# Kernel tuning notes

Measured on AMD Instinct MI355X. Metric: run time of the kernel, lower is better.

## Reference

```python
import jax, jax.numpy as jnp
import numpy as np

B, N, E, ITERS = 8, 1024, 10, 5


def _xavier(key, shape):
    fan_in, fan_out = shape[1], shape[0]
    std = float(np.sqrt(2.0 / (fan_in + fan_out)))
    return jax.random.normal(key, shape, dtype=jnp.float32) * std


def setup_inputs() -> dict:
    key = jax.random.key(0)
    ks = jax.random.split(key, 10)
    return {
        "features": jax.random.uniform(ks[0], (B, N), dtype=jnp.float32),
        "weights": jax.random.uniform(ks[1], (B, N, N), dtype=jnp.float32),
        "adjacency": jax.random.uniform(ks[2], (B, N, N), dtype=jnp.float32),
        # torch Linear(in, out) weight has shape (out, in); y = x @ W.T
        "w_selected": _xavier(ks[3], (E, 1)),
        "w_nbpriors": _xavier(ks[4], (E, E)),
        "w_nbweights": _xavier(ks[5], (E, E)),
        "w_nbweights_ew": _xavier(ks[6], (E, 1)),
        "w_q_reduc": _xavier(ks[7], (1, 2 * E)),
        "w_q_allembed": _xavier(ks[8], (E, E)),
        "w_q_action": _xavier(ks[9], (E, E)),
    }


def reference(features, weights, adjacency, w_selected, w_nbpriors,
              w_nbweights, w_nbweights_ew, w_q_reduc, w_q_allembed, w_q_action):
    b, n = features.shape
    e = w_selected.shape[0]
    # v_selected = Linear(1,E)(features[...,None]) -> outer product with (E,) vector
    v_selected = features[:, :, None] * w_selected[:, 0]            # [B,N,E]
    # relu(Linear(1,E)(weights[...,None])), then sum over dim=1 (source nodes)
    w_exp = jax.nn.relu(weights[:, :, :, None] * w_nbweights_ew[:, 0])  # [B,N,N,E]
    v_weights = jnp.einsum('bje,fe->bjf', jnp.sum(w_exp, axis=1), w_nbweights)  # [B,N,E]
    base = v_selected + v_weights

    embeddings = jnp.zeros((b, n, e), dtype=features.dtype)
    for _ in range(ITERS):
        v_priors = jnp.einsum('bij,bje->bie', adjacency, embeddings)  # [B,N,E]
        v_priors = jnp.einsum('bie,fe->bif', v_priors, w_nbpriors)
        embeddings = jax.nn.relu(base + v_priors)

    sumembed = jnp.einsum('bne,fe->bf', embeddings, w_q_allembed)     # [B,E]
    sumembed = jnp.broadcast_to(sumembed[:, None, :], (b, n, e))
    peract = jnp.einsum('bne,fe->bnf', embeddings, w_q_action)        # [B,N,E]
    q_in = jnp.concatenate([sumembed, peract], axis=2)                # [B,N,2E]
    q_vals = jnp.einsum('bnk,ok->bno', q_in, w_q_reduc)[:, :, 0]      # [B,N]
    return q_vals, embeddings
```

## Files before the change

kernel.cpp:

```cpp
#include <hip/hip_runtime.h>

#define B 8
#define N 1024
#define E 10
#define GP 44
#define EMB_FLOATS (256 * GP)
#define EMB_F4 (EMB_FLOATS / 4)
#define NBLK 256
#define TPB 32
#define BAR_PAD 32

typedef float f32x4 __attribute__((ext_vector_type(4)));

__device__ __forceinline__ void batch_barrier(unsigned* cnt) {
    __syncthreads();
    if (threadIdx.x == 0) {
        __hip_atomic_fetch_add(cnt, 1u, __ATOMIC_RELAXED, __HIP_MEMORY_SCOPE_AGENT);
        while (__hip_atomic_load(cnt, __ATOMIC_RELAXED, __HIP_MEMORY_SCOPE_AGENT) < TPB)
            __builtin_amdgcn_s_sleep(2);
    }
    __syncthreads();
    asm volatile("" ::: "memory");
}

__device__ __forceinline__ void store_llc(float* p, float v) {
    __hip_atomic_store((unsigned*)p, __float_as_uint(v),
                       __ATOMIC_RELAXED, __HIP_MEMORY_SCOPE_AGENT);
}
__device__ __forceinline__ float load_llc(const float* p) {
    unsigned u = __hip_atomic_load((const unsigned*)p,
                                   __ATOMIC_RELAXED, __HIP_MEMORY_SCOPE_AGENT);
    return __uint_as_float(u);
}


__global__ __launch_bounds__(1024, 4)
void k_fused6(
    const float* __restrict__ W, const float* __restrict__ features,
    const float* __restrict__ w_sel, const float* __restrict__ w_nbw,
    const float* __restrict__ w_ew, const float* __restrict__ A,
    const float* __restrict__ Wp, const float* __restrict__ w_reduc,
    const float* __restrict__ w_all, const float* __restrict__ w_act,
    float* eA, float* eB,
    float* __restrict__ emb_out, float* __restrict__ qv,
    float* __restrict__ qpart, unsigned* __restrict__ bars)
{
    __shared__ float4 EmS[EMB_F4];
    __shared__ float vred[16][9][2 * E];
    __shared__ float WpS[E * E];
    __shared__ float gaS[E], gactS[E];
    __shared__ float vS[32 * E], qS[32 * E], qrow[32];
    __shared__ float qsumS;

    int bx = blockIdx.x, tid = threadIdx.x;
    int b = bx >> 5, tile = bx & 31;
    int i0 = tile * 32;
    int m = tid >> 6;
    int s = tid & 63;
    unsigned* mybars = bars + b * BAR_PAD;

    float Arf[2][4][4];
    {
        const float* Ab = A + ((size_t)(b * N) + i0 + m) * N + 4 * s;
#pragma unroll
        for (int k = 0; k < 2; ++k)
#pragma unroll
            for (int c = 0; c < 4; ++c) {
                float4 t = *(const float4*)(Ab + (size_t)(16 * k) * N + 256 * c);
                Arf[k][c][0] = t.x; Arf[k][c][1] = t.y;
                Arf[k][c][2] = t.z; Arf[k][c][3] = t.w;
            }
    }

    if (tid < E * E) WpS[tid] = Wp[tid];
    if (tid < E) {
        float sa = 0.f, sc = 0.f;
#pragma unroll
        for (int k = 0; k < E; ++k) {
            sa += w_reduc[k] * w_all[k * E + tid];
            sc += w_reduc[E + k] * w_act[k * E + tid];
        }
        gaS[tid] = sa;
        gactS[tid] = sc;
    }

    float b_reg = 0.f;
    {
        float* redPt = (float*)&EmS[0];
        float* redNt = redPt + 32 * 129;
        float* scol  = redNt + 32 * 129;
        int c4 = (tid & 7) * 4;
        int rg = tid >> 3;
        const float* wp = W + ((size_t)b * N + rg * 8) * N + i0 + c4;
        float4 sp = {0.f, 0.f, 0.f, 0.f}, sn = {0.f, 0.f, 0.f, 0.f};
#pragma unroll
        for (int i = 0; i < 8; ++i) {
            float4 ww = *(const float4*)(wp + (size_t)i * N);
            sp.x += fmaxf(ww.x, 0.f); sn.x += fmaxf(-ww.x, 0.f);
            sp.y += fmaxf(ww.y, 0.f); sn.y += fmaxf(-ww.y, 0.f);
            sp.z += fmaxf(ww.z, 0.f); sn.z += fmaxf(-ww.z, 0.f);
            sp.w += fmaxf(ww.w, 0.f); sn.w += fmaxf(-ww.w, 0.f);
        }
        redPt[(c4 + 0) * 129 + rg] = sp.x; redNt[(c4 + 0) * 129 + rg] = sn.x;
        redPt[(c4 + 1) * 129 + rg] = sp.y; redNt[(c4 + 1) * 129 + rg] = sn.y;
        redPt[(c4 + 2) * 129 + rg] = sp.z; redNt[(c4 + 2) * 129 + rg] = sn.z;
        redPt[(c4 + 3) * 129 + rg] = sp.w; redNt[(c4 + 3) * 129 + rg] = sn.w;
        __syncthreads();
        if (tid < 64) {
            int cc = tid & 31;
            const float* rp = (tid < 32) ? redPt : redNt;
            float t = 0.f;
#pragma unroll 8
            for (int g = 0; g < 128; ++g) t += rp[cc * 129 + g];
            scol[(tid >> 5) * 32 + cc] = t;
        }
        __syncthreads();
        if (tid < 32 * E) {
            int cc = tid / E, f = tid % E;
            float spc = scol[cc], snc = scol[32 + cc];
            float acc = features[(b << 10) + i0 + cc] * w_sel[f];
#pragma unroll
            for (int e = 0; e < E; ++e) {
                float ce = w_ew[e];
                float se = (ce > 0.f) ? ce * spc : (-ce) * snc;
                acc += w_nbw[f * E + e] * se;
            }
            b_reg = acc;
            int row = i0 + cc;
            store_llc(&eA[(size_t)b * EMB_FLOATS + (row >> 2) * GP + (row & 3) * E + f],
                      fmaxf(acc, 0.f));
        }
    }
    batch_barrier(&mybars[0]);

    float da = 0.f;
    for (int it = 0; it < 4; ++it) {
        const float* ein = (it & 1) ? (const float*)eB : (const float*)eA;
        float* eout = (it & 1) ? eA : eB;

        {
            const f32x4* src = (const f32x4*)ein + (size_t)b * EMB_F4;
            f32x4 t0, t1, t2 = {0.f, 0.f, 0.f, 0.f};
            asm volatile("global_load_dwordx4 %0, %1, off sc0 sc1"
                         : "=v"(t0) : "v"(src + tid) : "memory");
            asm volatile("global_load_dwordx4 %0, %1, off sc0 sc1"
                         : "=v"(t1) : "v"(src + tid + 1024) : "memory");
            if (tid < EMB_F4 - 2048)
                asm volatile("global_load_dwordx4 %0, %1, off sc0 sc1"
                             : "=v"(t2) : "v"(src + tid + 2048) : "memory");
            asm volatile("s_waitcnt vmcnt(0)" ::: "memory");
            __builtin_amdgcn_sched_barrier(0);
            ((f32x4*)EmS)[tid]        = t0;
            ((f32x4*)EmS)[tid + 1024] = t1;
            if (tid < EMB_F4 - 2048) ((f32x4*)EmS)[tid + 2048] = t2;
        }
        __syncthreads();

        float acc[2][E];
#pragma unroll
        for (int k = 0; k < 2; ++k)
#pragma unroll
            for (int e = 0; e < E; ++e) acc[k][e] = 0.f;

#pragma unroll
        for (int c = 0; c < 4; ++c) {
            float4 g4[10];
            const float4* gp = EmS + (size_t)(s + 64 * c) * (GP / 4);
#pragma unroll
            for (int t = 0; t < 10; ++t) g4[t] = gp[t];
            const float* g40 = (const float*)g4;
#pragma unroll
            for (int q = 0; q < 4; ++q)
#pragma unroll
                for (int k = 0; k < 2; ++k) {
                    float a = Arf[k][c][q];
#pragma unroll
                    for (int e = 0; e < E; ++e)
                        acc[k][e] += a * g40[q * E + e];
                }
        }

#pragma unroll
        for (int mask = 1; mask <= 4; mask <<= 1)
#pragma unroll
            for (int k = 0; k < 2; ++k)
#pragma unroll
                for (int e = 0; e < E; ++e)
                    acc[k][e] += __shfl_xor(acc[k][e], mask, 64);
        if ((s & 7) == 0)
#pragma unroll
            for (int k = 0; k < 2; ++k)
#pragma unroll
                for (int e = 0; e < E; ++e)
                    vred[m][s >> 3][k * E + e] = acc[k][e];
        __syncthreads();

        if (tid < 32 * E) {
            int r = tid / E, f = tid % E;
            int mm = r & 15, kk = r >> 4;
            float v[E];
#pragma unroll
            for (int e = 0; e < E; ++e) {
                float t = 0.f;
#pragma unroll
                for (int g = 0; g < 8; ++g) t += vred[mm][g][kk * E + e];
                v[e] = t;
            }
            float d = 0.f;
#pragma unroll
            for (int e = 0; e < E; ++e) d += v[e] * WpS[f * E + e];
            float r_out = fmaxf(b_reg + d, 0.f);
            if (it < 3) {
                int grow = i0 + r;
                store_llc(&eout[(size_t)b * EMB_FLOATS + (grow >> 2) * GP + (grow & 3) * E + f],
                          r_out);
            } else {
                size_t gi = (size_t)((b << 10) + i0 + r);
                emb_out[gi * E + f] = r_out;
                vS[tid] = r_out * gactS[f];
                qS[tid] = r_out * gaS[f];
            }
        }
        if (it < 3) batch_barrier(&mybars[(1 + it) * B * BAR_PAD]);
    }

    __syncthreads();
    if (tid < 32) {
        float dg = 0.f;
#pragma unroll
        for (int f = 0; f < E; ++f) {
            da += vS[tid * E + f];
            dg += qS[tid * E + f];
        }
        qrow[tid] = dg;
    }
    __syncthreads();
    if (tid == 0) {
        float t = 0.f;
#pragma unroll
        for (int r = 0; r < 32; ++r) t += qrow[r];
        store_llc(&qpart[bx], t);
    }
    batch_barrier(&mybars[4 * B * BAR_PAD]);

    if (tid < 32) {
        float t = load_llc(&qpart[(b << 5) + tid]);
#pragma unroll
        for (int mask = 1; mask < 32; mask <<= 1)
            t += __shfl_xor(t, mask, 32);
        if (tid == 0) qsumS = t;
    }
    __syncthreads();
    if (tid < 32) qv[(b << 10) + i0 + tid] = da + qsumS;
}

__global__
__attribute__((amdgpu_flat_work_group_size(1024, 1024)))
__attribute__((amdgpu_waves_per_eu(4, 4)))
void k_fused7(
    const float* __restrict__ W, const float* __restrict__ features,
    const float* __restrict__ w_sel, const float* __restrict__ w_nbw,
    const float* __restrict__ w_ew, const float* __restrict__ A,
    const float* __restrict__ Wp, const float* __restrict__ w_reduc,
    const float* __restrict__ w_all, const float* __restrict__ w_act,
    float* eA, float* eB,
    float* __restrict__ emb_out, float* __restrict__ qv,
    float* __restrict__ qpart, unsigned* __restrict__ bars)
{
    __shared__ float4 EmS[EMB_F4];
    __shared__ float vred[16][5][4 * E];
    __shared__ float WpS[E * E];
    __shared__ float gaS[E], gactS[E];
    __shared__ float vS[32 * E], qS[32 * E], qrow[32];
    __shared__ float qsumS;

    int bx = blockIdx.x, tid = threadIdx.x;
    int b = bx >> 5, tile = bx & 31;
    int i0 = tile * 32;
    int w = tid >> 6;
    int s = tid & 63;
    int rs = tid >> 7;
    int jg = tid & 127;
    unsigned* mybars = bars + b * BAR_PAD;

    float Arf[4][2][4];
    {
        const float* Ab = A + ((size_t)(b * N) + i0 + (rs << 2)) * N + 4 * jg;
#pragma unroll
        for (int rr = 0; rr < 4; ++rr)
#pragma unroll
            for (int c = 0; c < 2; ++c) {
                float4 t = *(const float4*)(Ab + (size_t)rr * N + 512 * c);
                Arf[rr][c][0] = t.x; Arf[rr][c][1] = t.y;
                Arf[rr][c][2] = t.z; Arf[rr][c][3] = t.w;
            }
    }

    if (tid < E * E) WpS[tid] = Wp[tid];
    if (tid < E) {
        float sa = 0.f, sc = 0.f;
#pragma unroll
        for (int k = 0; k < E; ++k) {
            sa += w_reduc[k] * w_all[k * E + tid];
            sc += w_reduc[E + k] * w_act[k * E + tid];
        }
        gaS[tid] = sa;
        gactS[tid] = sc;
    }

    float b_reg = 0.f;
    {
        float* redPt = (float*)&EmS[0];
        float* redNt = redPt + 32 * 129;
        float* scol  = redNt + 32 * 129;
        int c4 = (tid & 7) * 4;
        int rg = tid >> 3;
        const float* wp = W + ((size_t)b * N + rg * 8) * N + i0 + c4;
        float4 sp = {0.f, 0.f, 0.f, 0.f}, sn = {0.f, 0.f, 0.f, 0.f};
#pragma unroll
        for (int i = 0; i < 8; ++i) {
            float4 ww = *(const float4*)(wp + (size_t)i * N);
            sp.x += fmaxf(ww.x, 0.f); sn.x += fmaxf(-ww.x, 0.f);
            sp.y += fmaxf(ww.y, 0.f); sn.y += fmaxf(-ww.y, 0.f);
            sp.z += fmaxf(ww.z, 0.f); sn.z += fmaxf(-ww.z, 0.f);
            sp.w += fmaxf(ww.w, 0.f); sn.w += fmaxf(-ww.w, 0.f);
        }
        redPt[(c4 + 0) * 129 + rg] = sp.x; redNt[(c4 + 0) * 129 + rg] = sn.x;
        redPt[(c4 + 1) * 129 + rg] = sp.y; redNt[(c4 + 1) * 129 + rg] = sn.y;
        redPt[(c4 + 2) * 129 + rg] = sp.z; redNt[(c4 + 2) * 129 + rg] = sn.z;
        redPt[(c4 + 3) * 129 + rg] = sp.w; redNt[(c4 + 3) * 129 + rg] = sn.w;
        __syncthreads();
        if (tid < 64) {
            int cc = tid & 31;
            const float* rp = (tid < 32) ? redPt : redNt;
            float t = 0.f;
#pragma unroll 8
            for (int g = 0; g < 128; ++g) t += rp[cc * 129 + g];
            scol[(tid >> 5) * 32 + cc] = t;
        }
        __syncthreads();
        if (tid < 32 * E) {
            int cc = tid / E, f = tid % E;
            float spc = scol[cc], snc = scol[32 + cc];
            float acc = features[(b << 10) + i0 + cc] * w_sel[f];
#pragma unroll
            for (int e = 0; e < E; ++e) {
                float ce = w_ew[e];
                float se = (ce > 0.f) ? ce * spc : (-ce) * snc;
                acc += w_nbw[f * E + e] * se;
            }
            b_reg = acc;
            int row = i0 + cc;
            store_llc(&eA[(size_t)b * EMB_FLOATS + (row >> 2) * GP + (row & 3) * E + f],
                      fmaxf(acc, 0.f));
        }
    }
    batch_barrier(&mybars[0]);

    float da = 0.f;
    for (int it = 0; it < 4; ++it) {
        const float* ein = (it & 1) ? (const float*)eB : (const float*)eA;
        float* eout = (it & 1) ? eA : eB;

        {
            const f32x4* src = (const f32x4*)ein + (size_t)b * EMB_F4;
            f32x4 t0, t1, t2 = {0.f, 0.f, 0.f, 0.f};
            asm volatile("global_load_dwordx4 %0, %1, off sc0 sc1"
                         : "=v"(t0) : "v"(src + tid) : "memory");
            asm volatile("global_load_dwordx4 %0, %1, off sc0 sc1"
                         : "=v"(t1) : "v"(src + tid + 1024) : "memory");
            if (tid < EMB_F4 - 2048)
                asm volatile("global_load_dwordx4 %0, %1, off sc0 sc1"
                             : "=v"(t2) : "v"(src + tid + 2048) : "memory");
            asm volatile("s_waitcnt vmcnt(0)" ::: "memory");
            __builtin_amdgcn_sched_barrier(0);
            ((f32x4*)EmS)[tid]        = t0;
            ((f32x4*)EmS)[tid + 1024] = t1;
            if (tid < EMB_F4 - 2048) ((f32x4*)EmS)[tid + 2048] = t2;
        }
        __syncthreads();

        float acc[4][E];
#pragma unroll
        for (int rr = 0; rr < 4; ++rr)
#pragma unroll
            for (int e = 0; e < E; ++e) acc[rr][e] = 0.f;

#pragma unroll
        for (int c = 0; c < 2; ++c) {
            const float4* gp = EmS + (size_t)(jg + 128 * c) * (GP / 4);
            {
                float4 g4a[5];
#pragma unroll
                for (int t = 0; t < 5; ++t) g4a[t] = gp[t];
                const float* ga = (const float*)g4a;
#pragma unroll
                for (int q = 0; q < 2; ++q)
#pragma unroll
                    for (int rr = 0; rr < 4; ++rr) {
                        float a = Arf[rr][c][q];
#pragma unroll
                        for (int e = 0; e < E; ++e)
                            acc[rr][e] += a * ga[q * E + e];
                    }
            }
            {
                float4 g4b[5];
#pragma unroll
                for (int t = 0; t < 5; ++t) g4b[t] = gp[5 + t];
                const float* gb = (const float*)g4b;
#pragma unroll
                for (int q = 0; q < 2; ++q)
#pragma unroll
                    for (int rr = 0; rr < 4; ++rr) {
                        float a = Arf[rr][c][q + 2];
#pragma unroll
                        for (int e = 0; e < E; ++e)
                            acc[rr][e] += a * gb[q * E + e];
                    }
            }
        }

#pragma unroll
        for (int mask = 1; mask <= 8; mask <<= 1)
#pragma unroll
            for (int rr = 0; rr < 4; ++rr)
#pragma unroll
                for (int e = 0; e < E; ++e)
                    acc[rr][e] += __shfl_xor(acc[rr][e], mask, 64);
        if ((s & 15) == 0)
#pragma unroll
            for (int rr = 0; rr < 4; ++rr)
#pragma unroll
                for (int e = 0; e < E; ++e)
                    vred[w][s >> 4][rr * E + e] = acc[rr][e];
        __syncthreads();

        if (tid < 32 * E) {
            int r = tid / E, f = tid % E;
            int prs = r >> 2, rr = r & 3;
            float v[E];
#pragma unroll
            for (int e = 0; e < E; ++e) {
                float t = 0.f;
#pragma unroll
                for (int h = 0; h < 2; ++h)
#pragma unroll
                    for (int p = 0; p < 4; ++p)
                        t += vred[(prs << 1) + h][p][rr * E + e];
                v[e] = t;
            }
            float d = 0.f;
#pragma unroll
            for (int e = 0; e < E; ++e) d += v[e] * WpS[f * E + e];
            float r_out = fmaxf(b_reg + d, 0.f);
            if (it < 3) {
                int grow = i0 + r;
                store_llc(&eout[(size_t)b * EMB_FLOATS + (grow >> 2) * GP + (grow & 3) * E + f],
                          r_out);
            } else {
                size_t gi = (size_t)((b << 10) + i0 + r);
                emb_out[gi * E + f] = r_out;
                vS[tid] = r_out * gactS[f];
                qS[tid] = r_out * gaS[f];
            }
        }
        if (it < 3) batch_barrier(&mybars[(1 + it) * B * BAR_PAD]);
    }

    __syncthreads();
    if (tid < 32) {
        float dg = 0.f;
#pragma unroll
        for (int f = 0; f < E; ++f) {
            da += vS[tid * E + f];
            dg += qS[tid * E + f];
        }
        qrow[tid] = dg;
    }
    __syncthreads();
    if (tid == 0) {
        float t = 0.f;
#pragma unroll
        for (int r = 0; r < 32; ++r) t += qrow[r];
        store_llc(&qpart[bx], t);
    }
    batch_barrier(&mybars[4 * B * BAR_PAD]);

    if (tid < 32) {
        float t = load_llc(&qpart[(b << 5) + tid]);
#pragma unroll
        for (int mask = 1; mask < 32; mask <<= 1)
            t += __shfl_xor(t, mask, 32);
        if (tid == 0) qsumS = t;
    }
    __syncthreads();
    if (tid < 32) qv[(b << 10) + i0 + tid] = da + qsumS;
}

extern "C" void kernel_launch(void* const* d_in, const int* in_sizes, int n_in,
                              void* d_out, int out_size, void* d_ws, size_t ws_size,
                              hipStream_t stream) {
    const float* features  = (const float*)d_in[0];
    const float* W         = (const float*)d_in[1];
    const float* adjacency = (const float*)d_in[2];
    const float* w_sel     = (const float*)d_in[3];
    const float* w_pri     = (const float*)d_in[4];
    const float* w_nbw     = (const float*)d_in[5];
    const float* w_ew      = (const float*)d_in[6];
    const float* w_reduc   = (const float*)d_in[7];
    const float* w_all     = (const float*)d_in[8];
    const float* w_act     = (const float*)d_in[9];

    float* out     = (float*)d_out;
    float* qv      = out;
    float* emb_out = out + B * N;

    float* ws      = (float*)d_ws;
    float* eA      = ws;
    float* eB      = eA + (size_t)B * EMB_FLOATS;
    float* qpart   = eB + (size_t)B * EMB_FLOATS;
    unsigned* bars = (unsigned*)(qpart + NBLK);

    static int use7 = -1;
    if (use7 < 0) {
        hipFuncAttributes fa{};
        use7 = 0;
        if (hipFuncGetAttributes(&fa, (const void*)k_fused7) == hipSuccess &&
            fa.localSizeBytes == 0 && fa.numRegs >= 96)
            use7 = 1;
    }

    hipMemsetAsync(bars, 0, 5 * B * BAR_PAD * sizeof(unsigned), stream);
    if (use7)
        k_fused7<<<NBLK, 1024, 0, stream>>>(W, features, w_sel, w_nbw, w_ew,
                                            adjacency, w_pri, w_reduc, w_all,
                                            w_act, eA, eB, emb_out, qv, qpart,
                                            bars);
    else
        k_fused6<<<NBLK, 1024, 0, stream>>>(W, features, w_sel, w_nbw, w_ew,
                                            adjacency, w_pri, w_reduc, w_all,
                                            w_act, eA, eB, emb_out, qv, qpart,
                                            bars);
}
```

Measured before the change: 146.8 us.

## Split fused GNN kernel into 512 blocks of 512 threads, 16 rows per block

The fused kernel is re-partitioned from 256 blocks of 1024 threads, each owning 32 rows, to 512 blocks of 512 threads, each owning 16 rows. Per-batch barriers now count 64 blocks, the embedding staging loop uses six loads per thread, and the final q reduction spans 64 partials. The aim is to spread the work across more CUs and cut per-block latency. In exchange, every block still reloads the full per-batch embedding each iteration and the grid barriers involve more participants. Parts of the body are hidden, so whether the adjacency register tiling fits the new shape cannot be checked.

```diff
diff --git a/kernel.cpp b/kernel.cpp
--- a/kernel.cpp
+++ b/kernel.cpp
@@ -6,17 +6,20 @@
 #define GP 44
 #define EMB_FLOATS (256 * GP)
 #define EMB_F4 (EMB_FLOATS / 4)
-#define NBLK 256
-#define TPB 32
 #define BAR_PAD 32
 
+#define NBLK6 256
+#define TPB6  32
+#define NBLK7 512
+#define TPB7  64
+
 typedef float f32x4 __attribute__((ext_vector_type(4)));
 
-__device__ __forceinline__ void batch_barrier(unsigned* cnt) {
+__device__ __forceinline__ void batch_barrier(unsigned* cnt, unsigned tpb) {
     __syncthreads();
     if (threadIdx.x == 0) {
         __hip_atomic_fetch_add(cnt, 1u, __ATOMIC_RELAXED, __HIP_MEMORY_SCOPE_AGENT);
-        while (__hip_atomic_load(cnt, __ATOMIC_RELAXED, __HIP_MEMORY_SCOPE_AGENT) < TPB)
+        while (__hip_atomic_load(cnt, __ATOMIC_RELAXED, __HIP_MEMORY_SCOPE_AGENT) < tpb)
             __builtin_amdgcn_s_sleep(2);
     }
     __syncthreads();
@@ -131,7 +134,7 @@
                       fmaxf(acc, 0.f));
         }
     }
-    batch_barrier(&mybars[0]);
+    batch_barrier(&mybars[0], TPB6);
 
     float da = 0.f;
     for (int it = 0; it < 4; ++it) {
@@ -221,7 +224,7 @@
                 qS[tid] = r_out * gaS[f];
             }
         }
-        if (it < 3) batch_barrier(&mybars[(1 + it) * B * BAR_PAD]);
+        if (it < 3) batch_barrier(&mybars[(1 + it) * B * BAR_PAD], TPB6);
     }
 
     __syncthreads();
@@ -241,7 +244,7 @@
         for (int r = 0; r < 32; ++r) t += qrow[r];
         store_llc(&qpart[bx], t);
     }
-    batch_barrier(&mybars[4 * B * BAR_PAD]);
+    batch_barrier(&mybars[4 * B * BAR_PAD], TPB6);
 
     if (tid < 32) {
         float t = load_llc(&qpart[(b << 5) + tid]);
@@ -254,10 +257,8 @@
     if (tid < 32) qv[(b << 10) + i0 + tid] = da + qsumS;
 }
 
-__global__
-__attribute__((amdgpu_flat_work_group_size(1024, 1024)))
-__attribute__((amdgpu_waves_per_eu(4, 4)))
-void k_fused7(
+__global__ __launch_bounds__(512, 4)
+void k_fused7x(
     const float* __restrict__ W, const float* __restrict__ features,
     const float* __restrict__ w_sel, const float* __restrict__ w_nbw,
     const float* __restrict__ w_ew, const float* __restrict__ A,
@@ -268,15 +269,15 @@
     float* __restrict__ qpart, unsigned* __restrict__ bars)
 {
     __shared__ float4 EmS[EMB_F4];
-    __shared__ float vred[16][5][4 * E];
+    __shared__ float vred[8][5][4 * E];
     __shared__ float WpS[E * E];
     __shared__ float gaS[E], gactS[E];
-    __shared__ float vS[32 * E], qS[32 * E], qrow[32];
+    __shared__ float vS[16 * E], qS[16 * E], qrow[16];
     __shared__ float qsumS;
 
     int bx = blockIdx.x, tid = threadIdx.x;
-    int b = bx >> 5, tile = bx & 31;
-    int i0 = tile * 32;
+    int b = bx >> 6, tile = bx & 63;
+    int i0 = tile * 16;
     int w = tid >> 6;
     int s = tid & 63;
     int rs = tid >> 7;
@@ -311,10 +312,10 @@
     float b_reg = 0.f;
     {
         float* redPt = (float*)&EmS[0];
-        float* redNt = redPt + 32 * 129;
-        float* scol  = redNt + 32 * 129;
-        int c4 = (tid & 7) * 4;
-        int rg = tid >> 3;
+        float* redNt = redPt + 16 * 129;
+        float* scol  = redNt + 16 * 129;
+        int c4 = (tid & 3) * 4;
+        int rg = tid >> 2;
         const float* wp = W + ((size_t)b * N + rg * 8) * N + i0 + c4;
         float4 sp = {0.f, 0.f, 0.f, 0.f}, sn = {0.f, 0.f, 0.f, 0.f};
 #pragma unroll
@@ -330,18 +331,18 @@
         redPt[(c4 + 2) * 129 + rg] = sp.z; redNt[(c4 + 2) * 129 + rg] = sn.z;
         redPt[(c4 + 3) * 129 + rg] = sp.w; redNt[(c4 + 3) * 129 + rg] = sn.w;
         __syncthreads();
-        if (tid < 64) {
-            int cc = tid & 31;
-            const float* rp = (tid < 32) ? redPt : redNt;
+        if (tid < 32) {
+            int cc = tid & 15;
+            const float* rp = (tid < 16) ? redPt : redNt;
             float t = 0.f;
 #pragma unroll 8
             for (int g = 0; g < 128; ++g) t += rp[cc * 129 + g];
-            scol[(tid >> 5) * 32 + cc] = t;
-        }
-        __syncthreads();
-        if (tid < 32 * E) {
+            scol[(tid >> 4) * 16 + cc] = t;
+        }
+        __syncthreads();
+        if (tid < 16 * E) {
             int cc = tid / E, f = tid % E;
-            float spc = scol[cc], snc = scol[32 + cc];
+            float spc = scol[cc], snc = scol[16 + cc];
             float acc = features[(b << 10) + i0 + cc] * w_sel[f];
 #pragma unroll
             for (int e = 0; e < E; ++e) {
@@ -355,7 +356,7 @@
                       fmaxf(acc, 0.f));
         }
     }
-    batch_barrier(&mybars[0]);
+    batch_barrier(&mybars[0], TPB7);
 
     float da = 0.f;
     for (int it = 0; it < 4; ++it) {
@@ -364,19 +365,20 @@
 
         {
             const f32x4* src = (const f32x4*)ein + (size_t)b * EMB_F4;
-            f32x4 t0, t1, t2 = {0.f, 0.f, 0.f, 0.f};
-            asm volatile("global_load_dwordx4 %0, %1, off sc0 sc1"
-                         : "=v"(t0) : "v"(src + tid) : "memory");
-            asm volatile("global_load_dwordx4 %0, %1, off sc0 sc1"
-                         : "=v"(t1) : "v"(src + tid + 1024) : "memory");
-            if (tid < EMB_F4 - 2048)
+            f32x4 tmp[5];
+            f32x4 t5 = {0.f, 0.f, 0.f, 0.f};
+#pragma unroll
+            for (int t = 0; t < 5; ++t)
                 asm volatile("global_load_dwordx4 %0, %1, off sc0 sc1"
-                             : "=v"(t2) : "v"(src + tid + 2048) : "memory");
+                             : "=v"(tmp[t]) : "v"(src + tid + 512 * t) : "memory");
+            if (tid < EMB_F4 - 2560)
+                asm volatile("global_load_dwordx4 %0, %1, off sc0 sc1"
+                             : "=v"(t5) : "v"(src + tid + 2560) : "memory");
             asm volatile("s_waitcnt vmcnt(0)" ::: "memory");
             __builtin_amdgcn_sched_barrier(0);
-            ((f32x4*)EmS)[tid]        = t0;
-            ((f32x4*)EmS)[tid + 1024] = t1;
-            if (tid < EMB_F4 - 2048) ((f32x4*)EmS)[tid + 2048] = t2;
+#pragma unroll
+            for (int t = 0; t < 5; ++t) ((f32x4*)EmS)[tid + 512 * t] = tmp[t];
+            if (tid < EMB_F4 - 2560) ((f32x4*)EmS)[tid + 2560] = t5;
         }
         __syncthreads();
 
@@ -436,7 +438,7 @@
                     vred[w][s >> 4][rr * E + e] = acc[rr][e];
         __syncthreads();
 
-        if (tid < 32 * E) {
+        if (tid < 16 * E) {
             int r = tid / E, f = tid % E;
             int prs = r >> 2, rr = r & 3;
             float v[E];
@@ -465,11 +467,11 @@
                 qS[tid] = r_out * gaS[f];
             }
         }
-        if (it < 3) batch_barrier(&mybars[(1 + it) * B * BAR_PAD]);
-    }
-
-    __syncthreads();
-    if (tid < 32) {
+        if (it < 3) batch_barrier(&mybars[(1 + it) * B * BAR_PAD], TPB7);
+    }
+
+    __syncthreads();
+    if (tid < 16) {
         float dg = 0.f;
 #pragma unroll
         for (int f = 0; f < E; ++f) {
@@ -482,20 +484,20 @@
     if (tid == 0) {
         float t = 0.f;
 #pragma unroll
-        for (int r = 0; r < 32; ++r) t += qrow[r];
+        for (int r = 0; r < 16; ++r) t += qrow[r];
         store_llc(&qpart[bx], t);
     }
-    batch_barrier(&mybars[4 * B * BAR_PAD]);
-
-    if (tid < 32) {
-        float t = load_llc(&qpart[(b << 5) + tid]);
-#pragma unroll
-        for (int mask = 1; mask < 32; mask <<= 1)
-            t += __shfl_xor(t, mask, 32);
+    batch_barrier(&mybars[4 * B * BAR_PAD], TPB7);
+
+    if (tid < 64) {
+        float t = load_llc(&qpart[(b << 6) + tid]);
+#pragma unroll
+        for (int mask = 1; mask < 64; mask <<= 1)
+            t += __shfl_xor(t, mask, 64);
         if (tid == 0) qsumS = t;
     }
     __syncthreads();
-    if (tid < 32) qv[(b << 10) + i0 + tid] = da + qsumS;
+    if (tid < 16) qv[(b << 10) + i0 + tid] = da + qsumS;
 }
 
 extern "C" void kernel_launch(void* const* d_in, const int* in_sizes, int n_in,
@@ -520,26 +522,26 @@
     float* eA      = ws;
     float* eB      = eA + (size_t)B * EMB_FLOATS;
     float* qpart   = eB + (size_t)B * EMB_FLOATS;
-    unsigned* bars = (unsigned*)(qpart + NBLK);
+    unsigned* bars = (unsigned*)(qpart + NBLK7);
 
     static int use7 = -1;
     if (use7 < 0) {
         hipFuncAttributes fa{};
         use7 = 0;
-        if (hipFuncGetAttributes(&fa, (const void*)k_fused7) == hipSuccess &&
-            fa.localSizeBytes == 0 && fa.numRegs >= 96)
+        if (hipFuncGetAttributes(&fa, (const void*)k_fused7x) == hipSuccess &&
+            fa.localSizeBytes == 0 && fa.numRegs >= 80 && fa.numRegs <= 128)
             use7 = 1;
     }
 
     hipMemsetAsync(bars, 0, 5 * B * BAR_PAD * sizeof(unsigned), stream);
     if (use7)
-        k_fused7<<<NBLK, 1024, 0, stream>>>(W, features, w_sel, w_nbw, w_ew,
-                                            adjacency, w_pri, w_reduc, w_all,
-                                            w_act, eA, eB, emb_out, qv, qpart,
-                                            bars);
+        k_fused7x<<<NBLK7, 512, 0, stream>>>(W, features, w_sel, w_nbw, w_ew,
+                                             adjacency, w_pri, w_reduc, w_all,
+                                             w_act, eA, eB, emb_out, qv, qpart,
+                                             bars);
     else
-        k_fused6<<<NBLK, 1024, 0, stream>>>(W, features, w_sel, w_nbw, w_ew,
-                                            adjacency, w_pri, w_reduc, w_all,
-                                            w_act, eA, eB, emb_out, qv, qpart,
-                                            bars);
+        k_fused6<<<NBLK6, 1024, 0, stream>>>(W, features, w_sel, w_nbw, w_ew,
+                                             adjacency, w_pri, w_reduc, w_all,
+                                             w_act, eA, eB, emb_out, qv, qpart,
+                                             bars);
 }
```

Result: no change. 147.5 us (+0.5%).

## Replace register-cached adjacency with L2-prefetched per-iteration loads in new kernel

Applied to the files above, without the earlier changes.

Adds k_fused8, which stops holding the 32x1024 adjacency tile in registers across iterations. It prefetches the tile once with a dummy read to warm the cache, then re-reads 2 rows x 16 columns per thread from global memory in each propagation iteration. The thread mapping changes to 2 rows per thread, with a cross-lane shuffle reduction over masks 16 and 32 plus a 16-way shared-memory reduction. This is meant to cut register pressure and shuffle work, at the cost of repeated global/L2 reads of A each iteration. The launch check now picks k_fused8 whenever its spill size is at most 8 bytes, and k_fused7 is removed.

```diff
diff --git a/kernel.cpp b/kernel.cpp
--- a/kernel.cpp
+++ b/kernel.cpp
@@ -6,9 +6,9 @@
 #define GP 44
 #define EMB_FLOATS (256 * GP)
 #define EMB_F4 (EMB_FLOATS / 4)
+#define BAR_PAD 32
 #define NBLK 256
 #define TPB 32
-#define BAR_PAD 32
 
 typedef float f32x4 __attribute__((ext_vector_type(4)));
 
@@ -33,6 +33,253 @@
     return __uint_as_float(u);
 }
 
+
+__global__ __launch_bounds__(1024, 4)
+void k_fused8(
+    const float* __restrict__ W, const float* __restrict__ features,
+    const float* __restrict__ w_sel, const float* __restrict__ w_nbw,
+    const float* __restrict__ w_ew, const float* __restrict__ A,
+    const float* __restrict__ Wp, const float* __restrict__ w_reduc,
+    const float* __restrict__ w_all, const float* __restrict__ w_act,
+    float* eA, float* eB,
+    float* __restrict__ emb_out, float* __restrict__ qv,
+    float* __restrict__ qpart, unsigned* __restrict__ bars)
+{
+    __shared__ float4 EmS[EMB_F4];
+    __shared__ float vredS[16 * 330];
+    __shared__ float WpS[E * E];
+    __shared__ float gaSh[E], gactS[E];
+    __shared__ float vS[32 * E], qS[32 * E], vS2[32 * E], qrow[32];
+    __shared__ float qsumS;
+
+    int bx = blockIdx.x, tid = threadIdx.x;
+    int b = bx >> 5, tile = bx & 31;
+    int i0 = tile * 32;
+    int w = tid >> 6;
+    int l = tid & 63;
+    int js = l >> 4;
+    int rs = l & 15;
+    unsigned* mybars = bars + b * BAR_PAD;
+
+    {
+        const f32x4* Aw = (const f32x4*)(A + ((size_t)(b << 10) + i0) * N) + tid;
+        f32x4 sink = {0.f, 0.f, 0.f, 0.f};
+#pragma unroll
+        for (int k = 0; k < 8; ++k) {
+            f32x4 t = Aw[k * 1024];
+            sink += t;
+        }
+        asm volatile("" :: "v"(sink.x), "v"(sink.y), "v"(sink.z), "v"(sink.w));
+    }
+
+    if (tid < E * E) WpS[tid] = Wp[tid];
+    if (tid < E) {
+        float sa = 0.f, sc = 0.f;
+#pragma unroll
+        for (int k = 0; k < E; ++k) {
+            sa += w_reduc[k] * w_all[k * E + tid];
+            sc += w_reduc[E + k] * w_act[k * E + tid];
+        }
+        gaSh[tid] = sa;
+        gactS[tid] = sc;
+    }
+
+    float b_reg = 0.f;
+    {
+        float* redPt = (float*)&EmS[0];
+        float* redNt = redPt + 32 * 129;
+        float* scol  = redNt + 32 * 129;
+        int c4 = (tid & 7) * 4;
+        int rg = tid >> 3;
+        const float* wp = W + ((size_t)b * N + rg * 8) * N + i0 + c4;
+        float4 sp = {0.f, 0.f, 0.f, 0.f}, sn = {0.f, 0.f, 0.f, 0.f};
+#pragma unroll
+        for (int i = 0; i < 8; ++i) {
+            float4 ww = *(const float4*)(wp + (size_t)i * N);
+            sp.x += fmaxf(ww.x, 0.f); sn.x += fmaxf(-ww.x, 0.f);
+            sp.y += fmaxf(ww.y, 0.f); sn.y += fmaxf(-ww.y, 0.f);
+            sp.z += fmaxf(ww.z, 0.f); sn.z += fmaxf(-ww.z, 0.f);
+            sp.w += fmaxf(ww.w, 0.f); sn.w += fmaxf(-ww.w, 0.f);
+        }
+        redPt[(c4 + 0) * 129 + rg] = sp.x; redNt[(c4 + 0) * 129 + rg] = sn.x;
+        redPt[(c4 + 1) * 129 + rg] = sp.y; redNt[(c4 + 1) * 129 + rg] = sn.y;
+        redPt[(c4 + 2) * 129 + rg] = sp.z; redNt[(c4 + 2) * 129 + rg] = sn.z;
+        redPt[(c4 + 3) * 129 + rg] = sp.w; redNt[(c4 + 3) * 129 + rg] = sn.w;
+        __syncthreads();
+        if (tid < 64) {
+            int cc = tid & 31;
+            const float* rp = (tid < 32) ? redPt : redNt;
+            float t = 0.f;
+#pragma unroll 8
+            for (int g = 0; g < 128; ++g) t += rp[cc * 129 + g];
+            scol[(tid >> 5) * 32 + cc] = t;
+        }
+        __syncthreads();
+        if (tid < 32 * E) {
+            int cc = tid / E, f = tid % E;
+            float spc = scol[cc], snc = scol[32 + cc];
+            float acc = features[(b << 10) + i0 + cc] * w_sel[f];
+#pragma unroll
+            for (int e = 0; e < E; ++e) {
+                float ce = w_ew[e];
+                float se = (ce > 0.f) ? ce * spc : (-ce) * snc;
+                acc += w_nbw[f * E + e] * se;
+            }
+            b_reg = acc;
+            int row = i0 + cc;
+            store_llc(&eA[(size_t)b * EMB_FLOATS + (row >> 2) * GP + (row & 3) * E + f],
+                      fmaxf(acc, 0.f));
+        }
+    }
+    batch_barrier(&mybars[0]);
+
+    const float* Ar0 = A + ((size_t)(b << 10) + i0 + 2 * rs) * N + 256 * js + 16 * w;
+    const float* Ar1 = Ar0 + N;
+    const float4* gp0 = EmS + (size_t)((js << 6) + (w << 2)) * (GP / 4);
+
+    float da = 0.f;
+    for (int it = 0; it < 4; ++it) {
+        const float* ein = (it & 1) ? (const float*)eB : (const float*)eA;
+        float* eout = (it & 1) ? eA : eB;
+
+        {
+            const f32x4* src = (const f32x4*)ein + (size_t)b * EMB_F4;
+            f32x4 t0, t1, t2 = {0.f, 0.f, 0.f, 0.f};
+            asm volatile("global_load_dwordx4 %0, %1, off sc0 sc1"
+                         : "=v"(t0) : "v"(src + tid) : "memory");
+            asm volatile("global_load_dwordx4 %0, %1, off sc0 sc1"
+                         : "=v"(t1) : "v"(src + tid + 1024) : "memory");
+            if (tid < EMB_F4 - 2048)
+                asm volatile("global_load_dwordx4 %0, %1, off sc0 sc1"
+                             : "=v"(t2) : "v"(src + tid + 2048) : "memory");
+            asm volatile("s_waitcnt vmcnt(0)" ::: "memory");
+            __builtin_amdgcn_sched_barrier(0);
+            ((f32x4*)EmS)[tid]        = t0;
+            ((f32x4*)EmS)[tid + 1024] = t1;
+            if (tid < EMB_F4 - 2048) ((f32x4*)EmS)[tid + 2048] = t2;
+        }
+        __syncthreads();
+
+        float acc0[E], acc1[E];
+#pragma unroll
+        for (int e = 0; e < E; ++e) { acc0[e] = 0.f; acc1[e] = 0.f; }
+
+#pragma unroll
+        for (int c = 0; c < 4; ++c) {
+            const float4* gp = gp0 + (size_t)c * (GP / 4);
+            float4 a0 = *(const float4*)(Ar0 + 4 * c);
+            float4 a1 = *(const float4*)(Ar1 + 4 * c);
+            {
+                float ga[20];
+                *(float4*)(ga + 0)  = gp[0];
+                *(float4*)(ga + 4)  = gp[1];
+                *(float4*)(ga + 8)  = gp[2];
+                *(float4*)(ga + 12) = gp[3];
+                *(float4*)(ga + 16) = gp[4];
+#pragma unroll
+                for (int e = 0; e < E; ++e) {
+                    acc0[e] += a0.x * ga[e];
+                    acc1[e] += a1.x * ga[e];
+                }
+#pragma unroll
+                for (int e = 0; e < E; ++e) {
+                    acc0[e] += a0.y * ga[10 + e];
+                    acc1[e] += a1.y * ga[10 + e];
+                }
+            }
+            {
+                float gb[20];
+                *(float4*)(gb + 0)  = gp[5];
+                *(float4*)(gb + 4)  = gp[6];
+                *(float4*)(gb + 8)  = gp[7];
+                *(float4*)(gb + 12) = gp[8];
+                *(float4*)(gb + 16) = gp[9];
+#pragma unroll
+                for (int e = 0; e < E; ++e) {
+                    acc0[e] += a0.z * gb[e];
+                    acc1[e] += a1.z * gb[e];
+                }
+#pragma unroll
+                for (int e = 0; e < E; ++e) {
+                    acc0[e] += a0.w * gb[10 + e];
+                    acc1[e] += a1.w * gb[10 + e];
+                }
+            }
+        }
+
+#pragma unroll
+        for (int mask = 16; mask <= 32; mask <<= 1)
+#pragma unroll
+            for (int e = 0; e < E; ++e) {
+                acc0[e] += __shfl_xor(acc0[e], mask, 64);
+                acc1[e] += __shfl_xor(acc1[e], mask, 64);
+            }
+        if (l < 16) {
+#pragma unroll
+            for (int e = 0; e < E; ++e) {
+                vredS[w * 330 + (2 * rs) * E + e]     = acc0[e];
+                vredS[w * 330 + (2 * rs + 1) * E + e] = acc1[e];
+            }
+        }
+        __syncthreads();
+
+        if (tid < 32 * E) {
+            float t = 0.f;
+#pragma unroll
+            for (int ww = 0; ww < 16; ++ww) t += vredS[ww * 330 + tid];
+            vS2[tid] = t;
+        }
+        __syncthreads();
+
+        if (tid < 32 * E) {
+            int r = tid / E, f = tid % E;
+            float d = 0.f;
+#pragma unroll
+            for (int e = 0; e < E; ++e) d += vS2[r * E + e] * WpS[f * E + e];
+            float r_out = fmaxf(b_reg + d, 0.f);
+            if (it < 3) {
+                int grow = i0 + r;
+                store_llc(&eout[(size_t)b * EMB_FLOATS + (grow >> 2) * GP + (grow & 3) * E + f],
+                          r_out);
+            } else {
+                size_t gi = (size_t)((b << 10) + i0 + r);
+                emb_out[gi * E + f] = r_out;
+                vS[tid] = r_out * gactS[f];
+                qS[tid] = r_out * gaSh[f];
+            }
+        }
+        if (it < 3) batch_barrier(&mybars[(1 + it) * B * BAR_PAD]);
+    }
+
+    __syncthreads();
+    if (tid < 32) {
+        float dg = 0.f;
+#pragma unroll
+        for (int f = 0; f < E; ++f) {
+            da += vS[tid * E + f];
+            dg += qS[tid * E + f];
+        }
+        qrow[tid] = dg;
+    }
+    __syncthreads();
+    if (tid == 0) {
+        float t = 0.f;
+#pragma unroll
+        for (int r = 0; r < 32; ++r) t += qrow[r];
+        store_llc(&qpart[bx], t);
+    }
+    batch_barrier(&mybars[4 * B * BAR_PAD]);
+
+    if (tid < 32) {
+        float t = load_llc(&qpart[(b << 5) + tid]);
+#pragma unroll
+        for (int mask = 1; mask < 32; mask <<= 1)
+            t += __shfl_xor(t, mask, 32);
+        if (tid == 0) qsumS = t;
+    }
+    __syncthreads();
+    if (tid < 32) qv[(b << 10) + i0 + tid] = da + qsumS;
+}
 
 __global__ __launch_bounds__(1024, 4)
 void k_fused6(
@@ -254,250 +501,6 @@
     if (tid < 32) qv[(b << 10) + i0 + tid] = da + qsumS;
 }
 
-__global__
-__attribute__((amdgpu_flat_work_group_size(1024, 1024)))
-__attribute__((amdgpu_waves_per_eu(4, 4)))
-void k_fused7(
-    const float* __restrict__ W, const float* __restrict__ features,
-    const float* __restrict__ w_sel, const float* __restrict__ w_nbw,
-    const float* __restrict__ w_ew, const float* __restrict__ A,
-    const float* __restrict__ Wp, const float* __restrict__ w_reduc,
-    const float* __restrict__ w_all, const float* __restrict__ w_act,
-    float* eA, float* eB,
-    float* __restrict__ emb_out, float* __restrict__ qv,
-    float* __restrict__ qpart, unsigned* __restrict__ bars)
-{
-    __shared__ float4 EmS[EMB_F4];
-    __shared__ float vred[16][5][4 * E];
-    __shared__ float WpS[E * E];
-    __shared__ float gaS[E], gactS[E];
-    __shared__ float vS[32 * E], qS[32 * E], qrow[32];
-    __shared__ float qsumS;
-
-    int bx = blockIdx.x, tid = threadIdx.x;
-    int b = bx >> 5, tile = bx & 31;
-    int i0 = tile * 32;
-    int w = tid >> 6;
-    int s = tid & 63;
-    int rs = tid >> 7;
-    int jg = tid & 127;
-    unsigned* mybars = bars + b * BAR_PAD;
-
-    float Arf[4][2][4];
-    {
-        const float* Ab = A + ((size_t)(b * N) + i0 + (rs << 2)) * N + 4 * jg;
-#pragma unroll
-        for (int rr = 0; rr < 4; ++rr)
-#pragma unroll
-            for (int c = 0; c < 2; ++c) {
-                float4 t = *(const float4*)(Ab + (size_t)rr * N + 512 * c);
-                Arf[rr][c][0] = t.x; Arf[rr][c][1] = t.y;
-                Arf[rr][c][2] = t.z; Arf[rr][c][3] = t.w;
-            }
-    }
-
-    if (tid < E * E) WpS[tid] = Wp[tid];
-    if (tid < E) {
-        float sa = 0.f, sc = 0.f;
-#pragma unroll
-        for (int k = 0; k < E; ++k) {
-            sa += w_reduc[k] * w_all[k * E + tid];
-            sc += w_reduc[E + k] * w_act[k * E + tid];
-        }
-        gaS[tid] = sa;
-        gactS[tid] = sc;
-    }
-
-    float b_reg = 0.f;
-    {
-        float* redPt = (float*)&EmS[0];
-        float* redNt = redPt + 32 * 129;
-        float* scol  = redNt + 32 * 129;
-        int c4 = (tid & 7) * 4;
-        int rg = tid >> 3;
-        const float* wp = W + ((size_t)b * N + rg * 8) * N + i0 + c4;
-        float4 sp = {0.f, 0.f, 0.f, 0.f}, sn = {0.f, 0.f, 0.f, 0.f};
-#pragma unroll
-        for (int i = 0; i < 8; ++i) {
-            float4 ww = *(const float4*)(wp + (size_t)i * N);
-            sp.x += fmaxf(ww.x, 0.f); sn.x += fmaxf(-ww.x, 0.f);
-            sp.y += fmaxf(ww.y, 0.f); sn.y += fmaxf(-ww.y, 0.f);
-            sp.z += fmaxf(ww.z, 0.f); sn.z += fmaxf(-ww.z, 0.f);
-            sp.w += fmaxf(ww.w, 0.f); sn.w += fmaxf(-ww.w, 0.f);
-        }
-        redPt[(c4 + 0) * 129 + rg] = sp.x; redNt[(c4 + 0) * 129 + rg] = sn.x;
-        redPt[(c4 + 1) * 129 + rg] = sp.y; redNt[(c4 + 1) * 129 + rg] = sn.y;
-        redPt[(c4 + 2) * 129 + rg] = sp.z; redNt[(c4 + 2) * 129 + rg] = sn.z;
-        redPt[(c4 + 3) * 129 + rg] = sp.w; redNt[(c4 + 3) * 129 + rg] = sn.w;
-        __syncthreads();
-        if (tid < 64) {
-            int cc = tid & 31;
-            const float* rp = (tid < 32) ? redPt : redNt;
-            float t = 0.f;
-#pragma unroll 8
-            for (int g = 0; g < 128; ++g) t += rp[cc * 129 + g];
-            scol[(tid >> 5) * 32 + cc] = t;
-        }
-        __syncthreads();
-        if (tid < 32 * E) {
-            int cc = tid / E, f = tid % E;
-            float spc = scol[cc], snc = scol[32 + cc];
-            float acc = features[(b << 10) + i0 + cc] * w_sel[f];
-#pragma unroll
-            for (int e = 0; e < E; ++e) {
-                float ce = w_ew[e];
-                float se = (ce > 0.f) ? ce * spc : (-ce) * snc;
-                acc += w_nbw[f * E + e] * se;
-            }
-            b_reg = acc;
-            int row = i0 + cc;
-            store_llc(&eA[(size_t)b * EMB_FLOATS + (row >> 2) * GP + (row & 3) * E + f],
-                      fmaxf(acc, 0.f));
-        }
-    }
-    batch_barrier(&mybars[0]);
-
-    float da = 0.f;
-    for (int it = 0; it < 4; ++it) {
-        const float* ein = (it & 1) ? (const float*)eB : (const float*)eA;
-        float* eout = (it & 1) ? eA : eB;
-
-        {
-            const f32x4* src = (const f32x4*)ein + (size_t)b * EMB_F4;
-            f32x4 t0, t1, t2 = {0.f, 0.f, 0.f, 0.f};
-            asm volatile("global_load_dwordx4 %0, %1, off sc0 sc1"
-                         : "=v"(t0) : "v"(src + tid) : "memory");
-            asm volatile("global_load_dwordx4 %0, %1, off sc0 sc1"
-                         : "=v"(t1) : "v"(src + tid + 1024) : "memory");
-            if (tid < EMB_F4 - 2048)
-                asm volatile("global_load_dwordx4 %0, %1, off sc0 sc1"
-                             : "=v"(t2) : "v"(src + tid + 2048) : "memory");
-            asm volatile("s_waitcnt vmcnt(0)" ::: "memory");
-            __builtin_amdgcn_sched_barrier(0);
-            ((f32x4*)EmS)[tid]        = t0;
-            ((f32x4*)EmS)[tid + 1024] = t1;
-            if (tid < EMB_F4 - 2048) ((f32x4*)EmS)[tid + 2048] = t2;
-        }
-        __syncthreads();
-
-        float acc[4][E];
-#pragma unroll
-        for (int rr = 0; rr < 4; ++rr)
-#pragma unroll
-            for (int e = 0; e < E; ++e) acc[rr][e] = 0.f;
-
-#pragma unroll
-        for (int c = 0; c < 2; ++c) {
-            const float4* gp = EmS + (size_t)(jg + 128 * c) * (GP / 4);
-            {
-                float4 g4a[5];
-#pragma unroll
-                for (int t = 0; t < 5; ++t) g4a[t] = gp[t];
-                const float* ga = (const float*)g4a;
-#pragma unroll
-                for (int q = 0; q < 2; ++q)
-#pragma unroll
-                    for (int rr = 0; rr < 4; ++rr) {
-                        float a = Arf[rr][c][q];
-#pragma unroll
-                        for (int e = 0; e < E; ++e)
-                            acc[rr][e] += a * ga[q * E + e];
-                    }
-            }
-            {
-                float4 g4b[5];
-#pragma unroll
-                for (int t = 0; t < 5; ++t) g4b[t] = gp[5 + t];
-                const float* gb = (const float*)g4b;
-#pragma unroll
-                for (int q = 0; q < 2; ++q)
-#pragma unroll
-                    for (int rr = 0; rr < 4; ++rr) {
-                        float a = Arf[rr][c][q + 2];
-#pragma unroll
-                        for (int e = 0; e < E; ++e)
-                            acc[rr][e] += a * gb[q * E + e];
-                    }
-            }
-        }
-
-#pragma unroll
-        for (int mask = 1; mask <= 8; mask <<= 1)
-#pragma unroll
-            for (int rr = 0; rr < 4; ++rr)
-#pragma unroll
-                for (int e = 0; e < E; ++e)
-                    acc[rr][e] += __shfl_xor(acc[rr][e], mask, 64);
-        if ((s & 15) == 0)
-#pragma unroll
-            for (int rr = 0; rr < 4; ++rr)
-#pragma unroll
-                for (int e = 0; e < E; ++e)
-                    vred[w][s >> 4][rr * E + e] = acc[rr][e];
-        __syncthreads();
-
-        if (tid < 32 * E) {
-            int r = tid / E, f = tid % E;
-            int prs = r >> 2, rr = r & 3;
-            float v[E];
-#pragma unroll
-            for (int e = 0; e < E; ++e) {
-                float t = 0.f;
-#pragma unroll
-                for (int h = 0; h < 2; ++h)
-#pragma unroll
-                    for (int p = 0; p < 4; ++p)
-                        t += vred[(prs << 1) + h][p][rr * E + e];
-                v[e] = t;
-            }
-            float d = 0.f;
-#pragma unroll
-            for (int e = 0; e < E; ++e) d += v[e] * WpS[f * E + e];
-            float r_out = fmaxf(b_reg + d, 0.f);
-            if (it < 3) {
-                int grow = i0 + r;
-                store_llc(&eout[(size_t)b * EMB_FLOATS + (grow >> 2) * GP + (grow & 3) * E + f],
-                          r_out);
-            } else {
-                size_t gi = (size_t)((b << 10) + i0 + r);
-                emb_out[gi * E + f] = r_out;
-                vS[tid] = r_out * gactS[f];
-                qS[tid] = r_out * gaS[f];
-            }
-        }
-        if (it < 3) batch_barrier(&mybars[(1 + it) * B * BAR_PAD]);
-    }
-
-    __syncthreads();
-    if (tid < 32) {
-        float dg = 0.f;
-#pragma unroll
-        for (int f = 0; f < E; ++f) {
-            da += vS[tid * E + f];
-            dg += qS[tid * E + f];
-        }
-        qrow[tid] = dg;
-    }
-    __syncthreads();
-    if (tid == 0) {
-        float t = 0.f;
-#pragma unroll
-        for (int r = 0; r < 32; ++r) t += qrow[r];
-        store_llc(&qpart[bx], t);
-    }
-    batch_barrier(&mybars[4 * B * BAR_PAD]);
-
-    if (tid < 32) {
-        float t = load_llc(&qpart[(b << 5) + tid]);
-#pragma unroll
-        for (int mask = 1; mask < 32; mask <<= 1)
-            t += __shfl_xor(t, mask, 32);
-        if (tid == 0) qsumS = t;
-    }
-    __syncthreads();
-    if (tid < 32) qv[(b << 10) + i0 + tid] = da + qsumS;
-}
-
 extern "C" void kernel_launch(void* const* d_in, const int* in_sizes, int n_in,
                               void* d_out, int out_size, void* d_ws, size_t ws_size,
                               hipStream_t stream) {
@@ -522,18 +525,18 @@
     float* qpart   = eB + (size_t)B * EMB_FLOATS;
     unsigned* bars = (unsigned*)(qpart + NBLK);
 
-    static int use7 = -1;
-    if (use7 < 0) {
+    static int use8 = -1;
+    if (use8 < 0) {
         hipFuncAttributes fa{};
-        use7 = 0;
-        if (hipFuncGetAttributes(&fa, (const void*)k_fused7) == hipSuccess &&
-            fa.localSizeBytes == 0 && fa.numRegs >= 96)
-            use7 = 1;
+        use8 = 0;
+        if (hipFuncGetAttributes(&fa, (const void*)k_fused8) == hipSuccess &&
+            fa.localSizeBytes <= 8)
+            use8 = 1;
     }
 
     hipMemsetAsync(bars, 0, 5 * B * BAR_PAD * sizeof(unsigned), stream);
-    if (use7)
-        k_fused7<<<NBLK, 1024, 0, stream>>>(W, features, w_sel, w_nbw, w_ew,
+    if (use8)
+        k_fused8<<<NBLK, 1024, 0, stream>>>(W, features, w_sel, w_nbw, w_ew,
                                             adjacency, w_pri, w_reduc, w_all,
                                             w_act, eA, eB, emb_out, qv, qpart,
                                             bars);
```

New measurement: 155.2 us. 1.06x slower.
